# Optimization experiments

Hardware: AMD Instinct MI355X
Metric: run time of the kernel (lower is better)

Reference implementation:

```python
import jax, jax.numpy as jnp
import numpy as np
import math

FACTOR = 5  # Informer 'factor' hyperparameter


def setup_inputs() -> dict:
    key = jax.random.key(0)
    B, L, H, D = 2, 2048, 16, 128
    k1, k2, k3, k4 = jax.random.split(key, 4)
    queries = jax.random.normal(k1, (B, L, H, D), jnp.float32)
    keys = jax.random.normal(k2, (B, L, H, D), jnp.float32)
    values = jax.random.normal(k3, (B, L, H, D), jnp.float32)
    sample_k = max(1, min(FACTOR * math.ceil(math.log(L)), L))  # u in the paper
    index_sample = jax.random.randint(k4, (L, sample_k), 0, L, dtype=jnp.int32)
    return {"queries": queries, "keys": keys, "values": values,
            "index_sample": index_sample}


def reference(queries, keys, values, index_sample):
    # queries/keys/values: [B, L, H, D] -> [B, H, L, D]
    Q = jnp.swapaxes(queries, 1, 2)
    K = jnp.swapaxes(keys, 1, 2)
    V = jnp.swapaxes(values, 1, 2)
    B, H, L_Q, D = Q.shape
    L_K = K.shape[2]
    # U_part = factor*ceil(ln L_K), clipped to L_K then to L_Q (n_top in _prob_QK)
    n_top = max(1, min(FACTOR * math.ceil(math.log(L_K)), L_K, L_Q))

    # --- _prob_QK: sampled scores ---
    # K_sample: [B, H, L_Q, sample_k, D] (same materialization as torch K_expand gather)
    K_sample = K[:, :, index_sample, :]
    Q_K_sample = jnp.einsum('bhqd,bhqsd->bhqs', Q, K_sample)
    # sparsity measure M: max - mean(over full L_K, per original torch code)
    M = Q_K_sample.max(axis=-1) - Q_K_sample.sum(axis=-1) / L_K  # [B,H,L_Q]
    _, M_top = jax.lax.top_k(M, n_top)  # [B,H,n_top]

    # gather top queries and compute their full attention rows
    Q_reduce = jnp.take_along_axis(Q, M_top[..., None], axis=2)  # [B,H,u,D]
    scores = jnp.einsum('bhud,bhkd->bhuk', Q_reduce, K)  # [B,H,u,L_K]
    scale = 1.0 / math.sqrt(D)
    scores = scores * scale

    # --- initial context (mask_flag=False): mean of V over keys ---
    context = jnp.broadcast_to(V.mean(axis=2, keepdims=True), (B, H, L_Q, D))

    # --- update context at top-query positions ---
    attn = jax.nn.softmax(scores, axis=-1)
    upd = jnp.einsum('bhuk,bhkd->bhud', attn, V)  # [B,H,u,D]
    bi = jnp.arange(B)[:, None, None]
    hi = jnp.arange(H)[None, :, None]
    context = context.at[bi, hi, M_top].set(upd)

    return jnp.swapaxes(context, 1, 2)  # [B, L_Q, H, D]
```

## Files before the change

kernel.cpp:

```cpp
#include <hip/hip_runtime.h>
#include <math.h>

#define B_    2
#define L_    2048
#define H_    16
#define D_    128
#define S_    40
#define NTOP_ 40
#define NCH_  8
#define CHK_  256
#define VCH_  32
#define CAND_ 512

#define SCALE_ 0.08838834764831843f

__device__ __forceinline__ unsigned int encf(float f) {
    unsigned int u = __float_as_uint(f);
    return (u & 0x80000000u) ? ~u : (u | 0x80000000u);
}
__device__ __forceinline__ float decf(unsigned int e) {
    unsigned int u = (e & 0x80000000u) ? (e ^ 0x80000000u) : ~e;
    return __uint_as_float(u);
}
__device__ __forceinline__ unsigned int bfpack(float a, float b) {
    unsigned int ua = __float_as_uint(a); ua = (ua + 0x7fffu + ((ua >> 16) & 1u)) >> 16;
    unsigned int ub = __float_as_uint(b); ub = (ub + 0x7fffu + ((ub >> 16) & 1u)) >> 16;
    return ua | (ub << 16);
}
__device__ __forceinline__ float lo16(unsigned int u) { return __uint_as_float(u << 16); }
__device__ __forceinline__ float hi16(unsigned int u) { return __uint_as_float(u & 0xffff0000u); }

__global__ __launch_bounds__(256) void k_pack_vpart(const float* __restrict__ K,
                                                    const float* __restrict__ V,
                                                    unsigned int* __restrict__ Kbf,
                                                    float* __restrict__ vpart) {
    const int bid = blockIdx.x, t = threadIdx.x;
    if (bid < 256) {
        const int bh = bid >> 3, kc = bid & 7;
        const int h = bh & 15, b = bh >> 4;
        const float4* K4 = (const float4*)K;
        uint2* out2 = (uint2*)Kbf;
        for (int j = 0; j < 32; ++j) {
            const int g = j * 256 + t;
            const int row = g >> 5, c = g & 31;
            const float4 v = K4[((size_t)(b * L_ + kc * 256 + row) * H_ + h) * 32 + c];
            out2[(size_t)(bh * L_ + kc * 256 + row) * 32 + c] =
                make_uint2(bfpack(v.x, v.y), bfpack(v.z, v.w));
        }
    } else {
        __shared__ float red[256];
        const int vbid = bid - 256;
        const int bh  = vbid >> 5;
        const int lc  = vbid & (VCH_ - 1);
        const int h   = bh & 15, b = bh >> 4;
        const int d   = t & (D_ - 1);
        const int sub = t >> 7;
        float acc = 0.0f;
        const int l0 = lc * (L_ / VCH_);
        for (int l = l0 + sub; l < l0 + L_ / VCH_; l += 2)
            acc += V[((size_t)(b * L_ + l) * H_ + h) * D_ + d];
        red[t] = acc;
        __syncthreads();
        if (t < D_) vpart[(size_t)vbid * D_ + t] = red[t] + red[t + 128];
    }
}

__global__ __launch_bounds__(256) void k1_sample_bf16(const float* __restrict__ Q,
                                                      const uint4* __restrict__ KB,
                                                      const int* __restrict__ idx,
                                                      float* __restrict__ M) {
    const int sb   = blockIdx.x;
    const int xcd  = sb & 7;
    const int li   = sb >> 3;
    const int bh   = (xcd << 2) + (li >> 9);
    const int rb   = li & 511;
    const int wave = threadIdx.x >> 6, lane = threadIdx.x & 63;
    const int q    = rb * 4 + wave;
    const int h    = bh & 15, b = bh >> 4;
    const int g    = lane >> 3, sub = lane & 7;

    const float4* Q4 = (const float4*)Q;
    const size_t rowQ = ((size_t)(b * L_ + q) * H_ + h) * 32;
    const int* ip = idx + q * S_;
    int kidx[5];
    #pragma unroll
    for (int s = 0; s < 5; ++s) kidx[s] = ip[s * 8 + g];

    const float4 qa0 = Q4[rowQ + 2 * sub];
    const float4 qa1 = Q4[rowQ + 2 * sub + 1];
    const float4 qb0 = Q4[rowQ + 16 + 2 * sub];
    const float4 qb1 = Q4[rowQ + 16 + 2 * sub + 1];

    uint4 kv[5][2];
    #pragma unroll
    for (int s = 0; s < 5; ++s) {
        const uint4* kr = KB + ((size_t)bh * L_ + kidx[s]) * 16;
        kv[s][0] = kr[sub];
        kv[s][1] = kr[8 + sub];
    }
    __builtin_amdgcn_sched_barrier(0);

    float smax = -INFINITY, ssum = 0.0f;
    #pragma unroll
    for (int s = 0; s < 5; ++s) {
        float p = 0.f;
        {
            const uint4 u = kv[s][0];
            p += qa0.x * lo16(u.x) + qa0.y * hi16(u.x) + qa0.z * lo16(u.y) + qa0.w * hi16(u.y);
            p += qa1.x * lo16(u.z) + qa1.y * hi16(u.z) + qa1.z * lo16(u.w) + qa1.w * hi16(u.w);
        }
        {
            const uint4 u = kv[s][1];
            p += qb0.x * lo16(u.x) + qb0.y * hi16(u.x) + qb0.z * lo16(u.y) + qb0.w * hi16(u.y);
            p += qb1.x * lo16(u.z) + qb1.y * hi16(u.z) + qb1.z * lo16(u.w) + qb1.w * hi16(u.w);
        }
        p += __shfl_xor(p, 1);
        p += __shfl_xor(p, 2);
        p += __shfl_xor(p, 4);
        smax = fmaxf(smax, p);
        ssum += p;
    }
    #pragma unroll
    for (int o = 8; o < 64; o <<= 1) {
        smax = fmaxf(smax, __shfl_xor(smax, o));
        ssum += __shfl_xor(ssum, o);
    }
    if (lane == 0) M[(size_t)bh * L_ + q] = smax - ssum * (1.0f / L_);
}

__global__ __launch_bounds__(256) void k1_sample_f32(const float* __restrict__ Q,
                                                     const float* __restrict__ K,
                                                     const int* __restrict__ idx,
                                                     float* __restrict__ M) {
    const int sb   = blockIdx.x;
    const int xcd  = sb & 7;
    const int li   = sb >> 3;
    const int bh   = (xcd << 2) + (li >> 9);
    const int rb   = li & 511;
    const int wave = threadIdx.x >> 6, lane = threadIdx.x & 63;
    const int q    = rb * 4 + wave;
    const int h    = bh & 15, b = bh >> 4;
    const int g    = lane >> 3, sub = lane & 7;

    const float4* Q4 = (const float4*)Q;
    const float4* K4 = (const float4*)K;
    const size_t rowQ = ((size_t)(b * L_ + q) * H_ + h) * 32;
    const size_t kbase = ((size_t)b * L_ * H_ + h) * 32 + sub;
    const int* ip = idx + q * S_;
    int kidx[5];
    #pragma unroll
    for (int s = 0; s < 5; ++s) kidx[s] = ip[s * 8 + g];
    const float4 qv0 = Q4[rowQ + 0 + sub];
    const float4 qv1 = Q4[rowQ + 8 + sub];
    const float4 qv2 = Q4[rowQ + 16 + sub];
    const float4 qv3 = Q4[rowQ + 24 + sub];
    float4 kv[5][4];
    #pragma unroll
    for (int s = 0; s < 5; ++s) {
        const float4* kb = K4 + kbase + (size_t)kidx[s] * (H_ * 32);
        kv[s][0] = kb[0]; kv[s][1] = kb[8]; kv[s][2] = kb[16]; kv[s][3] = kb[24];
    }
    __builtin_amdgcn_sched_barrier(0);
    float smax = -INFINITY, ssum = 0.0f;
    #pragma unroll
    for (int s = 0; s < 5; ++s) {
        float p = qv0.x * kv[s][0].x + qv0.y * kv[s][0].y + qv0.z * kv[s][0].z + qv0.w * kv[s][0].w
                + qv1.x * kv[s][1].x + qv1.y * kv[s][1].y + qv1.z * kv[s][1].z + qv1.w * kv[s][1].w
                + qv2.x * kv[s][2].x + qv2.y * kv[s][2].y + qv2.z * kv[s][2].z + qv2.w * kv[s][2].w
                + qv3.x * kv[s][3].x + qv3.y * kv[s][3].y + qv3.z * kv[s][3].z + qv3.w * kv[s][3].w;
        p += __shfl_xor(p, 1);
        p += __shfl_xor(p, 2);
        p += __shfl_xor(p, 4);
        smax = fmaxf(smax, p);
        ssum += p;
    }
    #pragma unroll
    for (int o = 8; o < 64; o <<= 1) {
        smax = fmaxf(smax, __shfl_xor(smax, o));
        ssum += __shfl_xor(ssum, o);
    }
    if (lane == 0) M[(size_t)bh * L_ + q] = smax - ssum * (1.0f / L_);
}

__global__ __launch_bounds__(1024) void k2_rank_refine_fill(const float* __restrict__ Mws,
                                                            const float* __restrict__ Q,
                                                            const float* __restrict__ K,
                                                            const int* __restrict__ idx,
                                                            const float* __restrict__ vpart,
                                                            int* __restrict__ topk,
                                                            float* __restrict__ out,
                                                            float delta) {
    const int bid = blockIdx.x, t = threadIdx.x;
    if (bid < 32) {
        __shared__ unsigned int ue[L_];
        __shared__ int hist[256], sscan[256];
        __shared__ int sh_chosen, sh_need, sh_nc;
        __shared__ int clist[CAND_];
        __shared__ float cMx[CAND_];
        __shared__ unsigned int cmaxe[CAND_];
        __shared__ float csum[CAND_];
        const int bh = bid, h = bh & 15, b = bh >> 4;
        const float* Mrow = Mws + (size_t)bh * L_;
        for (int i = t; i < L_; i += 1024) ue[i] = encf(Mrow[i]);
        if (t == 0) sh_nc = 0;
        __syncthreads();

        unsigned int prefix = 0; int need = NTOP_;
        for (int l = 3; l >= 0; --l) {
            if (t < 256) hist[t] = 0;
            __syncthreads();
            for (int i = t; i < L_; i += 1024) {
                const unsigned int u = ue[i];
                const bool match = (l == 3) || ((u >> (8 * (l + 1))) == prefix);
                if (match) atomicAdd(&hist[(u >> (8 * l)) & 255], 1);
            }
            __syncthreads();
            if (t < 256) sscan[t] = hist[t];
            __syncthreads();
            for (int off = 1; off < 256; off <<= 1) {
                int v = 0;
                if (t < 256 && t + off < 256) v = sscan[t + off];
                __syncthreads();
                if (t < 256) sscan[t] += v;
                __syncthreads();
            }
            if (t < 256) {
                const int above = sscan[t] - hist[t];
                if (above < need && need <= above + hist[t]) { sh_chosen = t; sh_need = need - above; }
            }
            __syncthreads();
            prefix = (prefix << 8) | (unsigned int)sh_chosen;
            need = sh_need;
            __syncthreads();
        }
        const unsigned int ethr = encf(decf(prefix) - delta);
        for (int i = t; i < L_; i += 1024) {
            if (ue[i] >= ethr) {
                const int p = atomicAdd(&sh_nc, 1);
                if (p < CAND_) clist[p] = i;
            }
        }
        __syncthreads();
        const int nc = min(sh_nc, CAND_);
        for (int i = t; i < CAND_; i += 1024) { cmaxe[i] = 0x007FFFFFu; csum[i] = 0.f; }
        __syncthreads();

        const float4* Q4 = (const float4*)Q;
        const float4* K4 = (const float4*)K;
        const int grp = t >> 3, sub = t & 7;
        for (int task = grp; task < nc * S_; task += 128) {
            const int ci = task / S_;
            const int s  = task - ci * S_;
            const int qq = clist[ci];
            const int ki = idx[qq * S_ + s];
            const float4* Kr = K4 + ((size_t)(b * L_ + ki) * H_ + h) * 32;
            const float4* Qr = Q4 + ((size_t)(b * L_ + qq) * H_ + h) * 32;
            float p = 0.f;
            #pragma unroll
            for (int qt2 = 0; qt2 < 4; ++qt2) {
                const float4 kv = Kr[qt2 * 8 + sub];
                const float4 qv = Qr[qt2 * 8 + sub];
                p += qv.x * kv.x + qv.y * kv.y + qv.z * kv.z + qv.w * kv.w;
            }
            p += __shfl_xor(p, 1);
            p += __shfl_xor(p, 2);
            p += __shfl_xor(p, 4);
            if (sub == 0) {
                atomicMax(&cmaxe[ci], encf(p));
                atomicAdd(&csum[ci], p);
            }
        }
        __syncthreads();
        if (t < nc) cMx[t] = decf(cmaxe[t]) - csum[t] * (1.0f / L_);
        __syncthreads();
        if (t < nc) {
            const float mi = cMx[t]; const int qi = clist[t];
            int rk = 0;
            for (int j = 0; j < nc; ++j) {
                const float mj = cMx[j];
                rk += (mj > mi) || (mj == mi && clist[j] < qi);
            }
            if (rk < NTOP_) topk[bh * NTOP_ + rk] = qi;
        }
    } else {
        __shared__ float red[1024];
        __shared__ float vmf[128];
        const int fb = bid - 32;
        const int bh = fb >> 4, sl = fb & 15;
        const int h = bh & 15, b = bh >> 4;
        const int d = t & 127, grp = t >> 7;
        float s = 0.f;
        #pragma unroll
        for (int c = grp * 4; c < grp * 4 + 4; ++c)
            s += vpart[(size_t)(bh * VCH_ + c) * D_ + d];
        red[t] = s;
        __syncthreads();
        if (t < 512) red[t] += red[t + 512];
        __syncthreads();
        if (t < 256) red[t] += red[t + 256];
        __syncthreads();
        if (t < 128) vmf[t] = (red[t] + red[t + 128]) * (1.0f / L_);
        __syncthreads();
        const float4 vm4 = *(const float4*)&vmf[(t & 31) * 4];
        float4* out4 = (float4*)out;
        const int q0 = sl * 128;
        #pragma unroll
        for (int k = 0; k < 4; ++k) {
            const int j = k * 1024 + t;
            const int r = j >> 5, c = j & 31;
            out4[((size_t)(b * L_ + q0 + r) * H_ + h) * 32 + c] = vm4;
        }
    }
}

__global__ __launch_bounds__(256) void k_scorepv(const float* __restrict__ Q,
                                                 const float* __restrict__ K,
                                                 const float* __restrict__ V,
                                                 const int* __restrict__ topk,
                                                 float* __restrict__ pmax,
                                                 float* __restrict__ psum,
                                                 float* __restrict__ pout) {
    __shared__ float Qs[20 * 132];
    __shared__ float S[20 * 260];
    __shared__ float mrow[20];
    __shared__ int   tq[20];
    const int bid = blockIdx.x;
    const int xcd = bid & 7;
    const int loc = bid >> 3;
    const int bh  = (xcd << 2) + (loc >> 4);
    const int sub16 = loc & 15;
    const int kc  = sub16 >> 1;
    const int uh  = sub16 & 1;
    const int h   = bh & 15, b = bh >> 4;
    const int t   = threadIdx.x;

    if (t < 20) tq[t] = topk[bh * NTOP_ + uh * 20 + t];
    __syncthreads();

    {
        const float4* Q4 = (const float4*)Q;
        #pragma unroll
        for (int it = 0; it < 3; ++it) {
            const int i = it * 256 + t;
            if (i < 640) {
                const int u = i >> 5, dc = i & 31;
                *(float4*)&Qs[u * 132 + dc * 4] =
                    Q4[((size_t)(b * L_ + tq[u]) * H_ + h) * 32 + dc];
            }
        }
    }
    __syncthreads();

    {
        const int kq4 = t >> 2, ug = t & 3;
        float acc[4][5];
        #pragma unroll
        for (int j = 0; j < 4; ++j)
            #pragma unroll
            for (int uu = 0; uu < 5; ++uu) acc[j][uu] = 0.f;
        const float4* Kb = (const float4*)K +
            ((size_t)(b * L_ + kc * CHK_ + kq4 * 4) * H_ + h) * 32;
        for (int dc = 0; dc < 32; ++dc) {
            float4 qv[5];
            #pragma unroll
            for (int uu = 0; uu < 5; ++uu)
                qv[uu] = *(const float4*)&Qs[(ug * 5 + uu) * 132 + dc * 4];
            #pragma unroll
            for (int j = 0; j < 4; ++j) {
                const float4 kv = Kb[(size_t)j * (H_ * 32) + dc];
                #pragma unroll
                for (int uu = 0; uu < 5; ++uu)
                    acc[j][uu] += qv[uu].x * kv.x + qv[uu].y * kv.y
                                + qv[uu].z * kv.z + qv[uu].w * kv.w;
            }
        }
        #pragma unroll
        for (int j = 0; j < 4; ++j)
            #pragma unroll
            for (int uu = 0; uu < 5; ++uu)
                S[(ug * 5 + uu) * 260 + kq4 * 4 + j] = acc[j][uu] * SCALE_;
    }
    __syncthreads();

    {
        const int w = t >> 6, lane = t & 63;
        #pragma unroll
        for (int uu = 0; uu < 5; ++uu) {
            const int u = w * 5 + uu;
            const float* Sr = S + u * 260;
            float v = fmaxf(fmaxf(Sr[lane], Sr[lane + 64]),
                            fmaxf(Sr[lane + 128], Sr[lane + 192]));
            #pragma unroll
            for (int o = 1; o < 64; o <<= 1) v = fmaxf(v, __shfl_xor(v, o, 64));
            if (lane == 0) mrow[u] = v;
        }
    }
    __syncthreads();

    #pragma unroll
    for (int u = 0; u < 20; ++u) S[u * 260 + t] = __expf(S[u * 260 + t] - mrow[u]);
    __syncthreads();

    {
        const int w = t >> 6, lane = t & 63;
        #pragma unroll
        for (int uu = 0; uu < 5; ++uu) {
            const int u = w * 5 + uu;
            const float* Sr = S + u * 260;
            float v = Sr[lane] + Sr[lane + 64] + Sr[lane + 128] + Sr[lane + 192];
            #pragma unroll
            for (int o = 1; o < 64; o <<= 1) v += __shfl_xor(v, o, 64);
            if (lane == 0) {
                psum[(bh * NCH_ + kc) * NTOP_ + uh * 20 + u] = v;
                pmax[(bh * NCH_ + kc) * NTOP_ + uh * 20 + u] = mrow[u];
            }
        }
    }

    {
        const int g = t >> 6, d2 = t & 63;
        const int u0 = g * 5;
        float accA[5], accB[5];
        #pragma unroll
        for (int uu = 0; uu < 5; ++uu) { accA[uu] = 0.f; accB[uu] = 0.f; }
        const float2* Vb = (const float2*)(V + ((size_t)(b * L_ + kc * CHK_) * H_ + h) * D_) + d2;
        for (int kq = 0; kq < CHK_ / 4; ++kq) {
            float2 v0 = Vb[(size_t)(kq * 4 + 0) * (H_ * D_ / 2)];
            float2 v1 = Vb[(size_t)(kq * 4 + 1) * (H_ * D_ / 2)];
            float2 v2 = Vb[(size_t)(kq * 4 + 2) * (H_ * D_ / 2)];
            float2 v3 = Vb[(size_t)(kq * 4 + 3) * (H_ * D_ / 2)];
            #pragma unroll
            for (int uu = 0; uu < 5; ++uu) {
                const float4 p = *(const float4*)&S[(u0 + uu) * 260 + kq * 4];
                accA[uu] += p.x * v0.x + p.y * v1.x + p.z * v2.x + p.w * v3.x;
                accB[uu] += p.x * v0.y + p.y * v1.y + p.z * v2.y + p.w * v3.y;
            }
        }
        float* pb = pout + (((size_t)(bh * NCH_ + kc)) * NTOP_ + uh * 20 + u0) * D_ + d2 * 2;
        #pragma unroll
        for (int uu = 0; uu < 5; ++uu)
            *(float2*)&pb[(size_t)uu * D_] = make_float2(accA[uu], accB[uu]);
    }
}

__global__ __launch_bounds__(128) void k_comb(const float* __restrict__ pmax,
                                              const float* __restrict__ psum,
                                              const float* __restrict__ pout,
                                              const int* __restrict__ topk,
                                              float* __restrict__ out) {
    const int bid = blockIdx.x;
    const int bh  = bid / NTOP_;
    const int u   = bid - bh * NTOP_;
    const int h   = bh & 15, b = bh >> 4;
    const int t   = threadIdx.x;

    float pm[NCH_];
    float M = -INFINITY;
    #pragma unroll
    for (int c = 0; c < NCH_; ++c) {
        pm[c] = pmax[(bh * NCH_ + c) * NTOP_ + u];
        M = fmaxf(M, pm[c]);
    }
    float ssum = 0.0f, o = 0.0f;
    #pragma unroll
    for (int c = 0; c < NCH_; ++c) {
        const float w = __expf(pm[c] - M);
        ssum += psum[(bh * NCH_ + c) * NTOP_ + u] * w;
        o += pout[((size_t)(bh * NCH_ + c) * NTOP_ + u) * D_ + t] * w;
    }
    const int qi = topk[bh * NTOP_ + u];
    out[((size_t)(b * L_ + qi) * H_ + h) * D_ + t] = o / ssum;
}

extern "C" void kernel_launch(void* const* d_in, const int* in_sizes, int n_in,
                              void* d_out, int out_size, void* d_ws, size_t ws_size,
                              hipStream_t stream) {
    const float* Q  = (const float*)d_in[0];
    const float* K  = (const float*)d_in[1];
    const float* V  = (const float*)d_in[2];
    const int* idx  = (const int*)d_in[3];
    float* out      = (float*)d_out;

    char* ws = (char*)d_ws;
    size_t off = 0;
    float* Mws   = (float*)(ws + off); off += (size_t)65536 * 4;
    float* vpart = (float*)(ws + off); off += (size_t)1024 * 128 * 4;
    int*   topk  = (int*)(ws + off);   off += 1280 * 4;
    float* pmax  = (float*)(ws + off); off += (size_t)256 * 40 * 4;
    float* psum  = (float*)(ws + off); off += (size_t)256 * 40 * 4;
    float* pout  = (float*)(ws + off); off += (size_t)256 * 40 * 128 * 4;
    unsigned int* Kbf = (unsigned int*)(ws + off);
    const size_t kbf_bytes = (size_t)32 * L_ * D_ * 2;
    const bool use_bf16 = (ws_size >= off + kbf_bytes);

    if (use_bf16) {
        hipLaunchKernelGGL(k_pack_vpart, dim3(1280), dim3(256), 0, stream, K, V, Kbf, vpart);
        hipLaunchKernelGGL(k1_sample_bf16, dim3(16384), dim3(256), 0, stream,
                           Q, (const uint4*)Kbf, idx, Mws);
    } else {
        hipLaunchKernelGGL(k_pack_vpart, dim3(1280), dim3(256), 0, stream, K, V, Kbf, vpart);
        hipLaunchKernelGGL(k1_sample_f32, dim3(16384), dim3(256), 0, stream,
                           Q, K, idx, Mws);
    }
    hipLaunchKernelGGL(k2_rank_refine_fill, dim3(32 + 512), dim3(1024), 0, stream,
                       Mws, Q, K, idx, vpart, topk, out, use_bf16 ? 2.0f : 0.01f);
    hipLaunchKernelGGL(k_scorepv, dim3(512), dim3(256), 0, stream,
                       Q, K, V, topk, pmax, psum, pout);
    hipLaunchKernelGGL(k_comb, dim3(1280), dim3(128), 0, stream,
                       pmax, psum, pout, topk, out);
}
```

Before: 138.2 us.

## Switch sampled-score K copy to fp16 with fdot2 and move V-mean into sample kernel

Packs K into fp16 instead of bf16 and computes the sampled Q·K scores with packed fp16 dot2 instructions, which need fewer ALU ops than the bf16 unpack-and-multiply sequence. The V column-sum partials move out of the pack kernel and into extra blocks of the sampling kernel, so the pack kernel is smaller and the V reduction can overlap with sampling. The refine margin for the candidate-ranking stage is tightened from 2.0 to 0.5 to match fp16's higher mantissa precision. The cost is Q also being rounded to fp16 and a risk of overflow or precision loss for large values. The tighter margin also risks ranking mismatches.

```diff
diff --git a/kernel.cpp b/kernel.cpp
--- a/kernel.cpp
+++ b/kernel.cpp
@@ -14,6 +14,25 @@
 
 #define SCALE_ 0.08838834764831843f
 
+typedef _Float16 half2_t __attribute__((ext_vector_type(2)));
+
+__device__ __forceinline__ half2_t as_h2(unsigned int u) {
+    union { unsigned int u; half2_t h; } x; x.u = u; return x.h;
+}
+__device__ __forceinline__ unsigned int h2pack(float a, float b) {
+    union { half2_t h; unsigned int u; } x;
+    x.h[0] = (_Float16)a; x.h[1] = (_Float16)b; return x.u;
+}
+#if __has_builtin(__builtin_amdgcn_fdot2)
+__device__ __forceinline__ float FDOT2(half2_t a, half2_t b, float c) {
+    return __builtin_amdgcn_fdot2(a, b, c, false);
+}
+#else
+__device__ __forceinline__ float FDOT2(half2_t a, half2_t b, float c) {
+    return c + (float)a[0] * (float)b[0] + (float)a[1] * (float)b[1];
+}
+#endif
+
 __device__ __forceinline__ unsigned int encf(float f) {
     unsigned int u = __float_as_uint(f);
     return (u & 0x80000000u) ? ~u : (u | 0x80000000u);
@@ -22,34 +41,35 @@
     unsigned int u = (e & 0x80000000u) ? (e ^ 0x80000000u) : ~e;
     return __uint_as_float(u);
 }
-__device__ __forceinline__ unsigned int bfpack(float a, float b) {
-    unsigned int ua = __float_as_uint(a); ua = (ua + 0x7fffu + ((ua >> 16) & 1u)) >> 16;
-    unsigned int ub = __float_as_uint(b); ub = (ub + 0x7fffu + ((ub >> 16) & 1u)) >> 16;
-    return ua | (ub << 16);
-}
-__device__ __forceinline__ float lo16(unsigned int u) { return __uint_as_float(u << 16); }
-__device__ __forceinline__ float hi16(unsigned int u) { return __uint_as_float(u & 0xffff0000u); }
-
-__global__ __launch_bounds__(256) void k_pack_vpart(const float* __restrict__ K,
-                                                    const float* __restrict__ V,
-                                                    unsigned int* __restrict__ Kbf,
-                                                    float* __restrict__ vpart) {
+
+__global__ __launch_bounds__(256) void kpack(const float* __restrict__ K,
+                                             unsigned int* __restrict__ Kf) {
     const int bid = blockIdx.x, t = threadIdx.x;
-    if (bid < 256) {
-        const int bh = bid >> 3, kc = bid & 7;
-        const int h = bh & 15, b = bh >> 4;
-        const float4* K4 = (const float4*)K;
-        uint2* out2 = (uint2*)Kbf;
-        for (int j = 0; j < 32; ++j) {
-            const int g = j * 256 + t;
-            const int row = g >> 5, c = g & 31;
-            const float4 v = K4[((size_t)(b * L_ + kc * 256 + row) * H_ + h) * 32 + c];
-            out2[(size_t)(bh * L_ + kc * 256 + row) * 32 + c] =
-                make_uint2(bfpack(v.x, v.y), bfpack(v.z, v.w));
-        }
-    } else {
+    const int bh = bid >> 3, kc = bid & 7;
+    const int h = bh & 15, b = bh >> 4;
+    const float4* K4 = (const float4*)K;
+    uint2* out2 = (uint2*)Kf;
+    for (int j = 0; j < 32; ++j) {
+        const int g = j * 256 + t;
+        const int row = g >> 5, c = g & 31;
+        const float4 v = K4[((size_t)(b * L_ + kc * 256 + row) * H_ + h) * 32 + c];
+        out2[(size_t)(bh * L_ + kc * 256 + row) * 32 + c] =
+            make_uint2(h2pack(v.x, v.y), h2pack(v.z, v.w));
+    }
+}
+
+__global__ __launch_bounds__(256) void k1_sample_f16(const float* __restrict__ Q,
+                                                     const uint4* __restrict__ KF,
+                                                     const float* __restrict__ V,
+                                                     const int* __restrict__ idx,
+                                                     float* __restrict__ M,
+                                                     float* __restrict__ vpart) {
+    const int bid = blockIdx.x;
+    const int t   = threadIdx.x;
+
+    if (bid < 1024) {
         __shared__ float red[256];
-        const int vbid = bid - 256;
+        const int vbid = bid;
         const int bh  = vbid >> 5;
         const int lc  = vbid & (VCH_ - 1);
         const int h   = bh & 15, b = bh >> 4;
@@ -62,19 +82,15 @@
         red[t] = acc;
         __syncthreads();
         if (t < D_) vpart[(size_t)vbid * D_ + t] = red[t] + red[t + 128];
-    }
-}
-
-__global__ __launch_bounds__(256) void k1_sample_bf16(const float* __restrict__ Q,
-                                                      const uint4* __restrict__ KB,
-                                                      const int* __restrict__ idx,
-                                                      float* __restrict__ M) {
-    const int sb   = blockIdx.x;
+        return;
+    }
+
+    const int sb   = bid - 1024;
     const int xcd  = sb & 7;
     const int li   = sb >> 3;
     const int bh   = (xcd << 2) + (li >> 9);
     const int rb   = li & 511;
-    const int wave = threadIdx.x >> 6, lane = threadIdx.x & 63;
+    const int wave = t >> 6, lane = t & 63;
     const int q    = rb * 4 + wave;
     const int h    = bh & 15, b = bh >> 4;
     const int g    = lane >> 3, sub = lane & 7;
@@ -94,26 +110,34 @@
     uint4 kv[5][2];
     #pragma unroll
     for (int s = 0; s < 5; ++s) {
-        const uint4* kr = KB + ((size_t)bh * L_ + kidx[s]) * 16;
+        const uint4* kr = KF + ((size_t)bh * L_ + kidx[s]) * 16;
         kv[s][0] = kr[sub];
         kv[s][1] = kr[8 + sub];
     }
     __builtin_amdgcn_sched_barrier(0);
 
+    half2_t qh[8];
+    qh[0][0] = (_Float16)qa0.x; qh[0][1] = (_Float16)qa0.y;
+    qh[1][0] = (_Float16)qa0.z; qh[1][1] = (_Float16)qa0.w;
+    qh[2][0] = (_Float16)qa1.x; qh[2][1] = (_Float16)qa1.y;
+    qh[3][0] = (_Float16)qa1.z; qh[3][1] = (_Float16)qa1.w;
+    qh[4][0] = (_Float16)qb0.x; qh[4][1] = (_Float16)qb0.y;
+    qh[5][0] = (_Float16)qb0.z; qh[5][1] = (_Float16)qb0.w;
+    qh[6][0] = (_Float16)qb1.x; qh[6][1] = (_Float16)qb1.y;
+    qh[7][0] = (_Float16)qb1.z; qh[7][1] = (_Float16)qb1.w;
+
     float smax = -INFINITY, ssum = 0.0f;
     #pragma unroll
     for (int s = 0; s < 5; ++s) {
         float p = 0.f;
-        {
-            const uint4 u = kv[s][0];
-            p += qa0.x * lo16(u.x) + qa0.y * hi16(u.x) + qa0.z * lo16(u.y) + qa0.w * hi16(u.y);
-            p += qa1.x * lo16(u.z) + qa1.y * hi16(u.z) + qa1.z * lo16(u.w) + qa1.w * hi16(u.w);
-        }
-        {
-            const uint4 u = kv[s][1];
-            p += qb0.x * lo16(u.x) + qb0.y * hi16(u.x) + qb0.z * lo16(u.y) + qb0.w * hi16(u.y);
-            p += qb1.x * lo16(u.z) + qb1.y * hi16(u.z) + qb1.z * lo16(u.w) + qb1.w * hi16(u.w);
-        }
+        p = FDOT2(qh[0], as_h2(kv[s][0].x), p);
+        p = FDOT2(qh[1], as_h2(kv[s][0].y), p);
+        p = FDOT2(qh[2], as_h2(kv[s][0].z), p);
+        p = FDOT2(qh[3], as_h2(kv[s][0].w), p);
+        p = FDOT2(qh[4], as_h2(kv[s][1].x), p);
+        p = FDOT2(qh[5], as_h2(kv[s][1].y), p);
+        p = FDOT2(qh[6], as_h2(kv[s][1].z), p);
+        p = FDOT2(qh[7], as_h2(kv[s][1].w), p);
         p += __shfl_xor(p, 1);
         p += __shfl_xor(p, 2);
         p += __shfl_xor(p, 4);
@@ -130,14 +154,35 @@
 
 __global__ __launch_bounds__(256) void k1_sample_f32(const float* __restrict__ Q,
                                                      const float* __restrict__ K,
+                                                     const float* __restrict__ V,
                                                      const int* __restrict__ idx,
-                                                     float* __restrict__ M) {
-    const int sb   = blockIdx.x;
+                                                     float* __restrict__ M,
+                                                     float* __restrict__ vpart) {
+    const int bid = blockIdx.x;
+    const int t   = threadIdx.x;
+    if (bid < 1024) {
+        __shared__ float red[256];
+        const int vbid = bid;
+        const int bh  = vbid >> 5;
+        const int lc  = vbid & (VCH_ - 1);
+        const int h   = bh & 15, b = bh >> 4;
+        const int d   = t & (D_ - 1);
+        const int sub = t >> 7;
+        float acc = 0.0f;
+        const int l0 = lc * (L_ / VCH_);
+        for (int l = l0 + sub; l < l0 + L_ / VCH_; l += 2)
+            acc += V[((size_t)(b * L_ + l) * H_ + h) * D_ + d];
+        red[t] = acc;
+        __syncthreads();
+        if (t < D_) vpart[(size_t)vbid * D_ + t] = red[t] + red[t + 128];
+        return;
+    }
+    const int sb   = bid - 1024;
     const int xcd  = sb & 7;
     const int li   = sb >> 3;
     const int bh   = (xcd << 2) + (li >> 9);
     const int rb   = li & 511;
-    const int wave = threadIdx.x >> 6, lane = threadIdx.x & 63;
+    const int wave = t >> 6, lane = t & 63;
     const int q    = rb * 4 + wave;
     const int h    = bh & 15, b = bh >> 4;
     const int g    = lane >> 3, sub = lane & 7;
@@ -489,21 +534,20 @@
     float* pmax  = (float*)(ws + off); off += (size_t)256 * 40 * 4;
     float* psum  = (float*)(ws + off); off += (size_t)256 * 40 * 4;
     float* pout  = (float*)(ws + off); off += (size_t)256 * 40 * 128 * 4;
-    unsigned int* Kbf = (unsigned int*)(ws + off);
-    const size_t kbf_bytes = (size_t)32 * L_ * D_ * 2;
-    const bool use_bf16 = (ws_size >= off + kbf_bytes);
-
-    if (use_bf16) {
-        hipLaunchKernelGGL(k_pack_vpart, dim3(1280), dim3(256), 0, stream, K, V, Kbf, vpart);
-        hipLaunchKernelGGL(k1_sample_bf16, dim3(16384), dim3(256), 0, stream,
-                           Q, (const uint4*)Kbf, idx, Mws);
+    unsigned int* Kf = (unsigned int*)(ws + off);
+    const size_t kf_bytes = (size_t)32 * L_ * D_ * 2;
+    const bool use_f16 = (ws_size >= off + kf_bytes);
+
+    if (use_f16) {
+        hipLaunchKernelGGL(kpack, dim3(256), dim3(256), 0, stream, K, Kf);
+        hipLaunchKernelGGL(k1_sample_f16, dim3(1024 + 16384), dim3(256), 0, stream,
+                           Q, (const uint4*)Kf, V, idx, Mws, vpart);
     } else {
-        hipLaunchKernelGGL(k_pack_vpart, dim3(1280), dim3(256), 0, stream, K, V, Kbf, vpart);
-        hipLaunchKernelGGL(k1_sample_f32, dim3(16384), dim3(256), 0, stream,
-                           Q, K, idx, Mws);
+        hipLaunchKernelGGL(k1_sample_f32, dim3(1024 + 16384), dim3(256), 0, stream,
+                           Q, K, V, idx, Mws, vpart);
     }
     hipLaunchKernelGGL(k2_rank_refine_fill, dim3(32 + 512), dim3(1024), 0, stream,
-                       Mws, Q, K, idx, vpart, topk, out, use_bf16 ? 2.0f : 0.01f);
+                       Mws, Q, K, idx, vpart, topk, out, use_f16 ? 0.5f : 0.01f);
     hipLaunchKernelGGL(k_scorepv, dim3(512), dim3(256), 0, stream,
                        Q, K, V, topk, pmax, psum, pout);
     hipLaunchKernelGGL(k_comb, dim3(1280), dim3(128), 0, stream,
```

New measurement: 127.4 us. 1.09x faster.
